# Kernel optimization log

Hardware: AMD Instinct MI355X
Metric: run time of the kernel (lower is better)

The kernel has to match this reference:

```python
import jax, jax.numpy as jnp
import numpy as np
import math

EPS = 1e-12
SQRT_2_OVER_PI = math.sqrt(2.0 / math.pi)

B, S, H = 8, 2048, 4096


def setup_inputs() -> dict:
    key = jax.random.key(0)
    k1, k2 = jax.random.split(key)
    x = jax.random.normal(k1, (B, S, H), dtype=jnp.float32)
    # Linear weight in torch layout [out, in]; scaled like nn.Linear default init
    W = jax.random.normal(k2, (H, H), dtype=jnp.float32) * (1.0 / math.sqrt(H))
    b = jnp.zeros((H,), dtype=jnp.float32)
    a2 = jnp.ones((H,), dtype=jnp.float32)   # LayerNorm scale
    b2 = jnp.zeros((H,), dtype=jnp.float32)  # LayerNorm shift
    return {"x": x, "W": W, "b": b, "a2": a2, "b2": b2}


def gelu_tanh(h):
    return 0.5 * h * (1.0 + jnp.tanh(SQRT_2_OVER_PI * (h + 0.044715 * h * h * h)))


def reference(x, W, b, a2, b2):
    # Linear: x @ W^T + b  (torch nn.Linear convention)
    h = jnp.einsum("bsh,oh->bso", x, W) + b
    g = gelu_tanh(h)
    # Custom LayerNorm (biased var, eps=1e-12): g*inv + (b2 - mean*inv)
    mean = jnp.mean(g, axis=-1, keepdims=True)
    var = jnp.mean(jnp.square(g - mean), axis=-1, keepdims=True)
    inv = jax.lax.rsqrt(var + EPS) * a2
    return g * inv + (b2 - mean * inv)
```

## Files before the change

### kernel.cpp

```cpp
#include <hip/hip_runtime.h>
#include <hip/hip_bf16.h>
#include <stdint.h>

#define M_TOTAL 16384
#define K_DIM   4096
#define N_DIM   4096
#define BM 128
#define BN 128
#define BK 32
#define NK (K_DIM / BK)

typedef unsigned short u16;
typedef __attribute__((ext_vector_type(4))) float  f32x4;
typedef __attribute__((ext_vector_type(8))) short  bf16x8;
typedef __attribute__((ext_vector_type(8))) unsigned short u16x8;

__device__ __forceinline__ u16 f2bf_rn(float f) {
    union { float f; uint32_t u; } x; x.f = f;
    uint32_t r = x.u + 0x7FFFu + ((x.u >> 16) & 1u);
    return (u16)(r >> 16);
}
__device__ __forceinline__ float bf2f(u16 s) {
    union { uint32_t u; float f; } x; x.u = ((uint32_t)s) << 16;
    return x.f;
}

#define ASYNC16(gp, lp) \
    __builtin_amdgcn_global_load_lds((const __attribute__((address_space(1))) void*)(gp), \
                                     (__attribute__((address_space(3))) void*)(lp), 16, 0, 0)

__global__ __launch_bounds__(256) void split_kernel(const float* __restrict__ in,
                                                    u16* __restrict__ hi,
                                                    u16* __restrict__ lo,
                                                    int nvec) {
    int i = blockIdx.x * 256 + threadIdx.x;
    if (i >= nvec) return;
    f32x4 v0 = ((const f32x4*)in)[2*i];
    f32x4 v1 = ((const f32x4*)in)[2*i + 1];
    u16x8 hv, lv;
#pragma unroll
    for (int j = 0; j < 8; ++j) {
        float f = (j < 4) ? v0[j] : v1[j - 4];
        u16 h = f2bf_rn(f);
        hv[j] = h;
        lv[j] = f2bf_rn(f - bf2f(h));
    }
    ((u16x8*)hi)[i] = hv;
    ((u16x8*)lo)[i] = lv;
}

__global__ __launch_bounds__(256, 2)
void gemm_gelu_kernel(const u16* __restrict__ xh, const u16* __restrict__ xl,
                      const u16* __restrict__ wh, const u16* __restrict__ wl,
                      const float* __restrict__ bias, float* __restrict__ out) {
    __shared__ __align__(16) u16 sAh[2][BM * BK];
    __shared__ __align__(16) u16 sAl[2][BM * BK];
    __shared__ __align__(16) u16 sBh[2][BN * BK];
    __shared__ __align__(16) u16 sBl[2][BN * BK];

    const int tid  = threadIdx.x;
    const int lane = tid & 63;
    const int wid  = tid >> 6;

    const int bid = blockIdx.x;
    const int c  = bid & 7;
    const int i  = bid >> 3;
    const int r  = i >> 8;
    const int j  = i & 255;
    const int bm = j >> 1;
    const int bn = (c << 2) + (r << 1) + (j & 1);

    const int row0 = bm * BM;
    const int col0 = bn * BN;

    const int c0 = tid;
    const int c1 = 256 + tid;
    const size_t aOff0 = (size_t)(row0 + (c0 >> 2)) * K_DIM + ((c0 & 3) << 3);
    const size_t aOff1 = (size_t)(row0 + (c1 >> 2)) * K_DIM + ((c1 & 3) << 3);
    const size_t bOff0 = (size_t)(col0 + (c0 >> 2)) * K_DIM + ((c0 & 3) << 3);
    const size_t bOff1 = (size_t)(col0 + (c1 >> 2)) * K_DIM + ((c1 & 3) << 3);

    auto STAGE = [&](int buf, int kt) {
        const size_t kofs = (size_t)kt * BK;
        ASYNC16(xh + aOff0 + kofs, sAh[buf] + c0 * 8);
        ASYNC16(xh + aOff1 + kofs, sAh[buf] + c1 * 8);
        ASYNC16(xl + aOff0 + kofs, sAl[buf] + c0 * 8);
        ASYNC16(xl + aOff1 + kofs, sAl[buf] + c1 * 8);
        ASYNC16(wh + bOff0 + kofs, sBh[buf] + c0 * 8);
        ASYNC16(wh + bOff1 + kofs, sBh[buf] + c1 * 8);
        ASYNC16(wl + bOff0 + kofs, sBl[buf] + c0 * 8);
        ASYNC16(wl + bOff1 + kofs, sBl[buf] + c1 * 8);
    };

    f32x4 acc[4][4] = {};
    const int wrow = (wid >> 1) << 6;
    const int wcol = (wid & 1) << 6;
    const int fr = lane & 15;
    const int kq = (lane >> 4) << 3;

    STAGE(0, 0);
    __syncthreads();

    for (int kt = 0; kt < NK; ++kt) {
        const int cur = kt & 1;
        if (kt + 1 < NK) STAGE(cur ^ 1, kt + 1);

        bf16x8 bh[4], bl[4];
#pragma unroll
        for (int n = 0; n < 4; ++n) {
            const int rr = wcol + n * 16 + fr;
            bh[n] = *(const bf16x8*)(sBh[cur] + rr * BK + kq);
            bl[n] = *(const bf16x8*)(sBl[cur] + rr * BK + kq);
        }
#pragma unroll
        for (int m = 0; m < 4; ++m) {
            const int rr = wrow + m * 16 + fr;
            bf16x8 ah = *(const bf16x8*)(sAh[cur] + rr * BK + kq);
            bf16x8 al = *(const bf16x8*)(sAl[cur] + rr * BK + kq);
#pragma unroll
            for (int n = 0; n < 4; ++n) {
                acc[m][n] = __builtin_amdgcn_mfma_f32_16x16x32_bf16(al, bh[n], acc[m][n], 0, 0, 0);
                acc[m][n] = __builtin_amdgcn_mfma_f32_16x16x32_bf16(ah, bl[n], acc[m][n], 0, 0, 0);
                acc[m][n] = __builtin_amdgcn_mfma_f32_16x16x32_bf16(ah, bh[n], acc[m][n], 0, 0, 0);
            }
        }

        __syncthreads();
    }

    const float SC = 0.7978845608028654f;
#pragma unroll
    for (int n = 0; n < 4; ++n) {
        const int col = col0 + wcol + n * 16 + (lane & 15);
        const float bc = bias[col];
#pragma unroll
        for (int m = 0; m < 4; ++m) {
            const int rbase = row0 + wrow + m * 16 + ((lane >> 4) << 2);
#pragma unroll
            for (int rr = 0; rr < 4; ++rr) {
                float h = acc[m][n][rr] + bc;
                float t = tanhf(SC * (h + 0.044715f * h * h * h));
                out[(size_t)(rbase + rr) * N_DIM + col] = 0.5f * h * (1.0f + t);
            }
        }
    }
}

__global__ __launch_bounds__(256)
void ln_kernel(float* __restrict__ out, const float* __restrict__ a2,
               const float* __restrict__ b2) {
    const int row = blockIdx.x;
    float* g = out + (size_t)row * N_DIM;
    const int tid = threadIdx.x;

    f32x4 v[4];
    float s = 0.f;
#pragma unroll
    for (int j = 0; j < 4; ++j) {
        v[j] = ((const f32x4*)g)[j * 256 + tid];
        s += v[j][0] + v[j][1] + v[j][2] + v[j][3];
    }
#pragma unroll
    for (int o = 32; o > 0; o >>= 1) s += __shfl_xor(s, o, 64);
    __shared__ float red[4];
    if ((tid & 63) == 0) red[tid >> 6] = s;
    __syncthreads();
    s = red[0] + red[1] + red[2] + red[3];
    const float mean = s * (1.0f / N_DIM);

    float q = 0.f;
#pragma unroll
    for (int j = 0; j < 4; ++j)
#pragma unroll
        for (int e = 0; e < 4; ++e) { float d = v[j][e] - mean; q += d * d; }
#pragma unroll
    for (int o = 32; o > 0; o >>= 1) q += __shfl_xor(q, o, 64);
    __shared__ float red2[4];
    if ((tid & 63) == 0) red2[tid >> 6] = q;
    __syncthreads();
    q = red2[0] + red2[1] + red2[2] + red2[3];
    const float var = q * (1.0f / N_DIM);
    const float inv = 1.0f / sqrtf(var + 1e-12f);

#pragma unroll
    for (int j = 0; j < 4; ++j) {
        f32x4 av = ((const f32x4*)a2)[j * 256 + tid];
        f32x4 bv = ((const f32x4*)b2)[j * 256 + tid];
        f32x4 o4;
#pragma unroll
        for (int e = 0; e < 4; ++e) o4[e] = (v[j][e] - mean) * inv * av[e] + bv[e];
        ((f32x4*)g)[j * 256 + tid] = o4;
    }
}

extern "C" void kernel_launch(void* const* d_in, const int* in_sizes, int n_in,
                              void* d_out, int out_size, void* d_ws, size_t ws_size,
                              hipStream_t stream) {
    const float* x  = (const float*)d_in[0];
    const float* W  = (const float*)d_in[1];
    const float* b  = (const float*)d_in[2];
    const float* a2 = (const float*)d_in[3];
    const float* b2 = (const float*)d_in[4];
    float* out = (float*)d_out;

    char* ws = (char*)d_ws;
    u16* xh = (u16*)(ws);
    u16* xl = (u16*)(ws + 134217728ull);
    u16* wh = (u16*)(ws + 268435456ull);
    u16* wl = (u16*)(ws + 301989888ull);

    split_kernel<<<8388608 / 256, 256, 0, stream>>>(x, xh, xl, 8388608);
    split_kernel<<<2097152 / 256, 256, 0, stream>>>(W, wh, wl, 2097152);

    gemm_gelu_kernel<<<4096, 256, 0, stream>>>(xh, xl, wh, wl, b, out);

    ln_kernel<<<M_TOTAL, 256, 0, stream>>>(out, a2, b2);
}
```

Before: 2.412 ms.

## Use 3-stage swizzled LDS pipeline with 512 threads per GEMM block

Reworks the split-bf16 GEMM kernel to use 512 threads (8 waves, each owning a 32x64 sub-tile) and merges the hi/lo shared-memory buffers into one XOR-swizzled 64-wide row per tile to avoid LDS bank conflicts. It replaces double buffering with a triple-buffered async pipeline that uses explicit vmcnt waits and a single barrier per k-step, keeping two loads in flight. The aim is better latency hiding and fewer LDS conflicts and barriers. In exchange, occupancy drops to one block per CU and each wave does less MFMA work per LDS read.

```diff
diff --git a/kernel.cpp b/kernel.cpp
--- a/kernel.cpp
+++ b/kernel.cpp
@@ -9,6 +9,7 @@
 #define BN 128
 #define BK 32
 #define NK (K_DIM / BK)
+#define THREADS 512
 
 typedef unsigned short u16;
 typedef __attribute__((ext_vector_type(4))) float  f32x4;
@@ -49,14 +50,12 @@
     ((u16x8*)lo)[i] = lv;
 }
 
-__global__ __launch_bounds__(256, 2)
+__global__ __launch_bounds__(THREADS, 1)
 void gemm_gelu_kernel(const u16* __restrict__ xh, const u16* __restrict__ xl,
                       const u16* __restrict__ wh, const u16* __restrict__ wl,
                       const float* __restrict__ bias, float* __restrict__ out) {
-    __shared__ __align__(16) u16 sAh[2][BM * BK];
-    __shared__ __align__(16) u16 sAl[2][BM * BK];
-    __shared__ __align__(16) u16 sBh[2][BN * BK];
-    __shared__ __align__(16) u16 sBl[2][BN * BK];
+    __shared__ __align__(16) u16 sA[3][BM * 64];
+    __shared__ __align__(16) u16 sB[3][BN * 64];
 
     const int tid  = threadIdx.x;
     const int lane = tid & 63;
@@ -73,60 +72,101 @@
     const int row0 = bm * BM;
     const int col0 = bn * BN;
 
-    const int c0 = tid;
-    const int c1 = 256 + tid;
-    const size_t aOff0 = (size_t)(row0 + (c0 >> 2)) * K_DIM + ((c0 & 3) << 3);
-    const size_t aOff1 = (size_t)(row0 + (c1 >> 2)) * K_DIM + ((c1 & 3) << 3);
-    const size_t bOff0 = (size_t)(col0 + (c0 >> 2)) * K_DIM + ((c0 & 3) << 3);
-    const size_t bOff1 = (size_t)(col0 + (c1 >> 2)) * K_DIM + ((c1 & 3) << 3);
-
-    auto STAGE = [&](int buf, int kt) {
-        const size_t kofs = (size_t)kt * BK;
-        ASYNC16(xh + aOff0 + kofs, sAh[buf] + c0 * 8);
-        ASYNC16(xh + aOff1 + kofs, sAh[buf] + c1 * 8);
-        ASYNC16(xl + aOff0 + kofs, sAl[buf] + c0 * 8);
-        ASYNC16(xl + aOff1 + kofs, sAl[buf] + c1 * 8);
-        ASYNC16(wh + bOff0 + kofs, sBh[buf] + c0 * 8);
-        ASYNC16(wh + bOff1 + kofs, sBh[buf] + c1 * 8);
-        ASYNC16(wl + bOff0 + kofs, sBl[buf] + c0 * 8);
-        ASYNC16(wl + bOff1 + kofs, sBl[buf] + c1 * 8);
-    };
-
-    f32x4 acc[4][4] = {};
-    const int wrow = (wid >> 1) << 6;
+    const u16* src0; const u16* src1; const u16* src2; const u16* src3;
+    int off0, off1, off2, off3;
+    {
+        int g, row, sp, sl;
+        g = tid;              row = g >> 3; sp = g & 7; sl = sp ^ (row & 7);
+        src0 = ((sl < 4) ? xh : xl) + (size_t)(row0 + row) * K_DIM + (sl & 3) * 8;
+        off0 = g * 8;
+        g = 512 + tid;        row = g >> 3; sp = g & 7; sl = sp ^ (row & 7);
+        src1 = ((sl < 4) ? xh : xl) + (size_t)(row0 + row) * K_DIM + (sl & 3) * 8;
+        off1 = g * 8;
+        g = tid;              row = g >> 3; sp = g & 7; sl = sp ^ (row & 7);
+        src2 = ((sl < 4) ? wh : wl) + (size_t)(col0 + row) * K_DIM + (sl & 3) * 8;
+        off2 = g * 8;
+        g = 512 + tid;        row = g >> 3; sp = g & 7; sl = sp ^ (row & 7);
+        src3 = ((sl < 4) ? wh : wl) + (size_t)(col0 + row) * K_DIM + (sl & 3) * 8;
+        off3 = g * 8;
+    }
+
+#define STAGE(buf, kt) { \
+        const size_t kofs = (size_t)(kt) * BK; \
+        ASYNC16(src0 + kofs, &sA[buf][off0]); \
+        ASYNC16(src1 + kofs, &sA[buf][off1]); \
+        ASYNC16(src2 + kofs, &sB[buf][off2]); \
+        ASYNC16(src3 + kofs, &sB[buf][off3]); \
+    }
+
+    const int wrow = (wid >> 1) << 5;
     const int wcol = (wid & 1) << 6;
-    const int fr = lane & 15;
-    const int kq = (lane >> 4) << 3;
+    const int fr  = lane & 15;
+    const int kq8 = lane >> 4;
+
+    f32x4 acc[2][4] = {};
 
     STAGE(0, 0);
-    __syncthreads();
-
-    for (int kt = 0; kt < NK; ++kt) {
-        const int cur = kt & 1;
-        if (kt + 1 < NK) STAGE(cur ^ 1, kt + 1);
-
-        bf16x8 bh[4], bl[4];
+    STAGE(1, 1);
+
+    for (int kt = 0; kt < NK - 1; ++kt) {
+        const int cur = kt % 3;
+        asm volatile("s_waitcnt vmcnt(4)" ::: "memory");
+        __builtin_amdgcn_s_barrier();
+        asm volatile("" ::: "memory");
+
+        if (kt + 2 < NK) STAGE((kt + 2) % 3, kt + 2);
+
+        bf16x8 ah[2], al[2], bh[4], bl[4];
+#pragma unroll
+        for (int m = 0; m < 2; ++m) {
+            const int rowA = wrow + m * 16 + fr;
+            ah[m] = *(const bf16x8*)(sA[cur] + rowA * 64 + ((kq8      ) ^ (rowA & 7)) * 8);
+            al[m] = *(const bf16x8*)(sA[cur] + rowA * 64 + ((kq8 | 4) ^ (rowA & 7)) * 8);
+        }
 #pragma unroll
         for (int n = 0; n < 4; ++n) {
-            const int rr = wcol + n * 16 + fr;
-            bh[n] = *(const bf16x8*)(sBh[cur] + rr * BK + kq);
-            bl[n] = *(const bf16x8*)(sBl[cur] + rr * BK + kq);
-        }
-#pragma unroll
-        for (int m = 0; m < 4; ++m) {
-            const int rr = wrow + m * 16 + fr;
-            bf16x8 ah = *(const bf16x8*)(sAh[cur] + rr * BK + kq);
-            bf16x8 al = *(const bf16x8*)(sAl[cur] + rr * BK + kq);
+            const int rowB = wcol + n * 16 + fr;
+            bh[n] = *(const bf16x8*)(sB[cur] + rowB * 64 + ((kq8      ) ^ (rowB & 7)) * 8);
+            bl[n] = *(const bf16x8*)(sB[cur] + rowB * 64 + ((kq8 | 4) ^ (rowB & 7)) * 8);
+        }
+#pragma unroll
+        for (int m = 0; m < 2; ++m)
 #pragma unroll
             for (int n = 0; n < 4; ++n) {
-                acc[m][n] = __builtin_amdgcn_mfma_f32_16x16x32_bf16(al, bh[n], acc[m][n], 0, 0, 0);
-                acc[m][n] = __builtin_amdgcn_mfma_f32_16x16x32_bf16(ah, bl[n], acc[m][n], 0, 0, 0);
-                acc[m][n] = __builtin_amdgcn_mfma_f32_16x16x32_bf16(ah, bh[n], acc[m][n], 0, 0, 0);
+                acc[m][n] = __builtin_amdgcn_mfma_f32_16x16x32_bf16(al[m], bh[n], acc[m][n], 0, 0, 0);
+                acc[m][n] = __builtin_amdgcn_mfma_f32_16x16x32_bf16(ah[m], bl[n], acc[m][n], 0, 0, 0);
+                acc[m][n] = __builtin_amdgcn_mfma_f32_16x16x32_bf16(ah[m], bh[n], acc[m][n], 0, 0, 0);
             }
-        }
-
-        __syncthreads();
-    }
+    }
+
+    {
+        const int cur = (NK - 1) % 3;
+        asm volatile("s_waitcnt vmcnt(0)" ::: "memory");
+        __builtin_amdgcn_s_barrier();
+        asm volatile("" ::: "memory");
+        bf16x8 ah[2], al[2], bh[4], bl[4];
+#pragma unroll
+        for (int m = 0; m < 2; ++m) {
+            const int rowA = wrow + m * 16 + fr;
+            ah[m] = *(const bf16x8*)(sA[cur] + rowA * 64 + ((kq8      ) ^ (rowA & 7)) * 8);
+            al[m] = *(const bf16x8*)(sA[cur] + rowA * 64 + ((kq8 | 4) ^ (rowA & 7)) * 8);
+        }
+#pragma unroll
+        for (int n = 0; n < 4; ++n) {
+            const int rowB = wcol + n * 16 + fr;
+            bh[n] = *(const bf16x8*)(sB[cur] + rowB * 64 + ((kq8      ) ^ (rowB & 7)) * 8);
+            bl[n] = *(const bf16x8*)(sB[cur] + rowB * 64 + ((kq8 | 4) ^ (rowB & 7)) * 8);
+        }
+#pragma unroll
+        for (int m = 0; m < 2; ++m)
+#pragma unroll
+            for (int n = 0; n < 4; ++n) {
+                acc[m][n] = __builtin_amdgcn_mfma_f32_16x16x32_bf16(al[m], bh[n], acc[m][n], 0, 0, 0);
+                acc[m][n] = __builtin_amdgcn_mfma_f32_16x16x32_bf16(ah[m], bl[n], acc[m][n], 0, 0, 0);
+                acc[m][n] = __builtin_amdgcn_mfma_f32_16x16x32_bf16(ah[m], bh[n], acc[m][n], 0, 0, 0);
+            }
+    }
+#undef STAGE
 
     const float SC = 0.7978845608028654f;
 #pragma unroll
@@ -134,7 +174,7 @@
         const int col = col0 + wcol + n * 16 + (lane & 15);
         const float bc = bias[col];
 #pragma unroll
-        for (int m = 0; m < 4; ++m) {
+        for (int m = 0; m < 2; ++m) {
             const int rbase = row0 + wrow + m * 16 + ((lane >> 4) << 2);
 #pragma unroll
             for (int rr = 0; rr < 4; ++rr) {
@@ -212,7 +252,7 @@
     split_kernel<<<8388608 / 256, 256, 0, stream>>>(x, xh, xl, 8388608);
     split_kernel<<<2097152 / 256, 256, 0, stream>>>(W, wh, wl, 2097152);
 
-    gemm_gelu_kernel<<<4096, 256, 0, stream>>>(xh, xl, wh, wl, b, out);
+    gemm_gelu_kernel<<<4096, THREADS, 0, stream>>>(xh, xl, wh, wl, b, out);
 
     ln_kernel<<<M_TOTAL, 256, 0, stream>>>(out, a2, b2);
 }
```

Result: slower. 3.153 ms (+30.7%).

## Interleave hi/lo tiles in XOR-swizzled LDS and use explicit vmcnt waits

Applied to the files above, without the earlier changes.

Merges the separate hi and lo shared-memory tiles into one 64-element-per-row buffer per operand, with an XOR swizzle on 16-byte chunks to avoid LDS bank conflicts on the MFMA fragment reads. The prefetch loop now issues the next stage, waits only until the current stage's async loads have landed (vmcnt(8)), then barriers, rather than relying on __syncthreads to drain every outstanding load. This is meant to cut bank conflicts and let the next tile's loads overlap with compute. Correctness now depends on the hand-counted vmcnt value matching the number of loads issued per stage.

```diff
diff --git a/kernel.cpp b/kernel.cpp
--- a/kernel.cpp
+++ b/kernel.cpp
@@ -53,10 +53,8 @@
 void gemm_gelu_kernel(const u16* __restrict__ xh, const u16* __restrict__ xl,
                       const u16* __restrict__ wh, const u16* __restrict__ wl,
                       const float* __restrict__ bias, float* __restrict__ out) {
-    __shared__ __align__(16) u16 sAh[2][BM * BK];
-    __shared__ __align__(16) u16 sAl[2][BM * BK];
-    __shared__ __align__(16) u16 sBh[2][BN * BK];
-    __shared__ __align__(16) u16 sBl[2][BN * BK];
+    __shared__ __align__(16) u16 sA[2][BM * 64];
+    __shared__ __align__(16) u16 sB[2][BN * 64];
 
     const int tid  = threadIdx.x;
     const int lane = tid & 63;
@@ -73,50 +71,58 @@
     const int row0 = bm * BM;
     const int col0 = bn * BN;
 
-    const int c0 = tid;
-    const int c1 = 256 + tid;
-    const size_t aOff0 = (size_t)(row0 + (c0 >> 2)) * K_DIM + ((c0 & 3) << 3);
-    const size_t aOff1 = (size_t)(row0 + (c1 >> 2)) * K_DIM + ((c1 & 3) << 3);
-    const size_t bOff0 = (size_t)(col0 + (c0 >> 2)) * K_DIM + ((c0 & 3) << 3);
-    const size_t bOff1 = (size_t)(col0 + (c1 >> 2)) * K_DIM + ((c1 & 3) << 3);
-
-    auto STAGE = [&](int buf, int kt) {
-        const size_t kofs = (size_t)kt * BK;
-        ASYNC16(xh + aOff0 + kofs, sAh[buf] + c0 * 8);
-        ASYNC16(xh + aOff1 + kofs, sAh[buf] + c1 * 8);
-        ASYNC16(xl + aOff0 + kofs, sAl[buf] + c0 * 8);
-        ASYNC16(xl + aOff1 + kofs, sAl[buf] + c1 * 8);
-        ASYNC16(wh + bOff0 + kofs, sBh[buf] + c0 * 8);
-        ASYNC16(wh + bOff1 + kofs, sBh[buf] + c1 * 8);
-        ASYNC16(wl + bOff0 + kofs, sBl[buf] + c0 * 8);
-        ASYNC16(wl + bOff1 + kofs, sBl[buf] + c1 * 8);
-    };
-
-    f32x4 acc[4][4] = {};
+    const u16* srcA[4]; const u16* srcB[4]; int offAB[4];
+#pragma unroll
+    for (int q = 0; q < 4; ++q) {
+        const int g = q * 256 + tid, row = g >> 3, sp = g & 7, sl = sp ^ (row & 7);
+        srcA[q] = ((sl < 4) ? xh : xl) + (size_t)(row0 + row) * K_DIM + (sl & 3) * 8;
+        srcB[q] = ((sl < 4) ? wh : wl) + (size_t)(col0 + row) * K_DIM + (sl & 3) * 8;
+        offAB[q] = g * 8;
+    }
+
+#define STAGE(buf, kt) { \
+        const size_t kofs = (size_t)(kt) * BK; \
+        _Pragma("unroll") \
+        for (int q = 0; q < 4; ++q) { \
+            ASYNC16(srcA[q] + kofs, &sA[buf][offAB[q]]); \
+            ASYNC16(srcB[q] + kofs, &sB[buf][offAB[q]]); \
+        } \
+    }
+
     const int wrow = (wid >> 1) << 6;
     const int wcol = (wid & 1) << 6;
-    const int fr = lane & 15;
-    const int kq = (lane >> 4) << 3;
+    const int fr  = lane & 15;
+    const int kq8 = lane >> 4;
+
+    f32x4 acc[4][4] = {};
 
     STAGE(0, 0);
-    __syncthreads();
 
     for (int kt = 0; kt < NK; ++kt) {
         const int cur = kt & 1;
-        if (kt + 1 < NK) STAGE(cur ^ 1, kt + 1);
+        if (kt + 1 < NK) {
+            STAGE(cur ^ 1, kt + 1);
+            asm volatile("s_waitcnt vmcnt(8)" ::: "memory");
+        } else {
+            asm volatile("s_waitcnt vmcnt(0)" ::: "memory");
+        }
+        __builtin_amdgcn_s_barrier();
+        asm volatile("" ::: "memory");
 
         bf16x8 bh[4], bl[4];
 #pragma unroll
         for (int n = 0; n < 4; ++n) {
-            const int rr = wcol + n * 16 + fr;
-            bh[n] = *(const bf16x8*)(sBh[cur] + rr * BK + kq);
-            bl[n] = *(const bf16x8*)(sBl[cur] + rr * BK + kq);
+            const int rowB = wcol + n * 16 + fr;
+            const u16* base = sB[cur] + rowB * 64;
+            bh[n] = *(const bf16x8*)(base + ((kq8      ) ^ (rowB & 7)) * 8);
+            bl[n] = *(const bf16x8*)(base + ((kq8 | 4) ^ (rowB & 7)) * 8);
         }
 #pragma unroll
         for (int m = 0; m < 4; ++m) {
-            const int rr = wrow + m * 16 + fr;
-            bf16x8 ah = *(const bf16x8*)(sAh[cur] + rr * BK + kq);
-            bf16x8 al = *(const bf16x8*)(sAl[cur] + rr * BK + kq);
+            const int rowA = wrow + m * 16 + fr;
+            const u16* baseA = sA[cur] + rowA * 64;
+            bf16x8 ah = *(const bf16x8*)(baseA + ((kq8      ) ^ (rowA & 7)) * 8);
+            bf16x8 al = *(const bf16x8*)(baseA + ((kq8 | 4) ^ (rowA & 7)) * 8);
 #pragma unroll
             for (int n = 0; n < 4; ++n) {
                 acc[m][n] = __builtin_amdgcn_mfma_f32_16x16x32_bf16(al, bh[n], acc[m][n], 0, 0, 0);
@@ -125,8 +131,10 @@
             }
         }
 
-        __syncthreads();
-    }
+        asm volatile("" ::: "memory");
+        __builtin_amdgcn_s_barrier();
+    }
+#undef STAGE
 
     const float SC = 0.7978845608028654f;
 #pragma unroll
```

After: 2.223 ms. 1.08x faster.
